# Kernel optimization log

Measured on AMD Instinct MI355X. Metric: run time of the kernel, lower is better.

## Reference

```python
import jax, jax.numpy as jnp
import numpy as np

N = 4096
IN_F = 128
OUT_F = 128
H = 4
D = OUT_F // H  # head_out = 32
SLOPE = 0.2
LN_EPS = 1e-5


def setup_inputs() -> dict:
    key = jax.random.key(0)
    k_x, k_adj, k_W, k_a = jax.random.split(key, 4)
    x = jax.random.normal(k_x, (N, IN_F), dtype=jnp.float32)
    adjacency = jax.random.randint(k_adj, (N, N), 0, 2).astype(jnp.bool_)
    # xavier-uniform-ish init scales
    w_std = float(np.sqrt(2.0 / (IN_F + H * D)))
    a_std = float(np.sqrt(2.0 / (H + 2 * D)))
    W = jax.random.normal(k_W, (H * D, IN_F), dtype=jnp.float32) * w_std  # torch Linear weight layout
    a = jax.random.normal(k_a, (H, 2 * D), dtype=jnp.float32) * a_std
    ln_gamma = jnp.ones((OUT_F,), dtype=jnp.float32)
    ln_beta = jnp.zeros((OUT_F,), dtype=jnp.float32)
    return {"x": x, "adjacency": adjacency, "W": W, "a": a,
            "ln_gamma": ln_gamma, "ln_beta": ln_beta}


def reference(x, adjacency, W, a, ln_gamma, ln_beta):
    # Wx: (N, H, D)
    Wx = (x @ W.T).reshape(N, H, D)
    # e[i,j,h] = leaky_relu( <Wx[i,h], a[h,:D]> + <Wx[j,h], a[h,D:]> )
    # (exact factorization of the original cat([Wx_i, Wx_j]) * a sum)
    alpha_i = jnp.einsum('nhd,hd->nh', Wx, a[:, :D])  # source/i term
    alpha_j = jnp.einsum('nhd,hd->nh', Wx, a[:, D:])  # neighbor/j term
    e = alpha_i[:, None, :] + alpha_j[None, :, :]      # (N, N, H)
    e = jnp.where(e >= 0, e, SLOPE * e)                # LeakyReLU
    e = jnp.where(adjacency[:, :, None], e, -jnp.inf)  # mask non-edges
    attn = jax.nn.softmax(e, axis=1)                   # softmax over j
    out = jnp.einsum('ijh,jhd->ihd', attn, Wx).reshape(N, H * D)
    y = out + x                                        # residual (dims match)
    mu = jnp.mean(y, axis=-1, keepdims=True)
    var = jnp.mean((y - mu) ** 2, axis=-1, keepdims=True)
    return ln_gamma * (y - mu) / jnp.sqrt(var + LN_EPS) + ln_beta
```

## Files before the change

### kernel.cpp

```cpp
#include <hip/hip_runtime.h>
#include <hip/hip_bf16.h>
#include <stdint.h>

#define NN 4096
#define SLOPE 0.2f
#define LOG2E 1.44269504088896340736f

typedef float f32x4 __attribute__((ext_vector_type(4)));
typedef short s16x8 __attribute__((ext_vector_type(8)));
typedef unsigned u32x4 __attribute__((ext_vector_type(4)));

static __device__ __forceinline__ unsigned f32_to_bf16_rne(float f) {
    unsigned u = __builtin_bit_cast(unsigned, f);
    return (u + 0x7FFFu + ((u >> 16) & 1u)) >> 16;
}

__global__ __launch_bounds__(256) void k01(const unsigned* __restrict__ adj_raw,
                                           const float* __restrict__ x,
                                           const float* __restrict__ W,
                                           const float* __restrict__ a,
                                           unsigned* __restrict__ bits,
                                           unsigned* __restrict__ wxb8,
                                           float* __restrict__ ai_s,
                                           float* __restrict__ ajT_s) {
    const int t = threadIdx.x;
    if (blockIdx.x < 2048) {
        __shared__ int s_i32;
        if (t == 0) {
            int all_small = 1;
            for (int i = 0; i < 32; ++i) all_small &= (adj_raw[i] <= 1u);
            s_i32 = all_small;
        }
        __syncthreads();
        const long o = (long)blockIdx.x * 256 + t;
        unsigned mm = 0;
        if (s_i32) {
            const u32x4* p = (const u32x4*)adj_raw + o * 8;
            #pragma unroll
            for (int g = 0; g < 8; ++g) {
                u32x4 v = p[g];
                mm |= (v.x & 1u) << (g * 4) | (v.y & 1u) << (g * 4 + 1) |
                      (v.z & 1u) << (g * 4 + 2) | (v.w & 1u) << (g * 4 + 3);
            }
        } else {
            const u32x4* p = (const u32x4*)adj_raw + o * 2;
            #pragma unroll
            for (int g = 0; g < 2; ++g) {
                u32x4 v = p[g];
                unsigned d[4] = {v.x, v.y, v.z, v.w};
                #pragma unroll
                for (int qq = 0; qq < 4; ++qq)
                    #pragma unroll
                    for (int b = 0; b < 4; ++b)
                        mm |= ((d[qq] >> (8 * b)) & 1u) << (g * 16 + qq * 4 + b);
            }
        }
        bits[o] = mm;
        return;
    }

    __shared__ unsigned short WL[128 * 136];
    __shared__ unsigned short XL[16 * 136];
    __shared__ float WxF[16 * 132];

    const int bid = blockIdx.x - 2048;
    const int i0 = bid * 16;

    for (int p4 = t; p4 < 4096; p4 += 256) {
        f32x4 w4 = *(const f32x4*)(W + 4 * p4);
        unsigned lo = f32_to_bf16_rne(w4.x) | (f32_to_bf16_rne(w4.y) << 16);
        unsigned hi = f32_to_bf16_rne(w4.z) | (f32_to_bf16_rne(w4.w) << 16);
        int c = (4 * p4) >> 7, k = (4 * p4) & 127;
        *(unsigned long long*)&WL[c * 136 + k] =
            (unsigned long long)lo | ((unsigned long long)hi << 32);
    }
    for (int p4 = t; p4 < 512; p4 += 256) {
        f32x4 x4 = *(const f32x4*)(x + (long)i0 * 128 + 4 * p4);
        unsigned lo = f32_to_bf16_rne(x4.x) | (f32_to_bf16_rne(x4.y) << 16);
        unsigned hi = f32_to_bf16_rne(x4.z) | (f32_to_bf16_rne(x4.w) << 16);
        int r = (4 * p4) >> 7, k = (4 * p4) & 127;
        *(unsigned long long*)&XL[r * 136 + k] =
            (unsigned long long)lo | ((unsigned long long)hi << 32);
    }
    __syncthreads();

    const int w = t >> 6, l = t & 63, m = l & 15, q = l >> 4;
    f32x4 acc0 = {0.f, 0.f, 0.f, 0.f}, acc1 = {0.f, 0.f, 0.f, 0.f};
    #pragma unroll
    for (int ks = 0; ks < 4; ++ks) {
        s16x8 af = *(const s16x8*)&XL[m * 136 + ks * 32 + q * 8];
        s16x8 b0 = *(const s16x8*)&WL[(w * 32 + m) * 136 + ks * 32 + q * 8];
        s16x8 b1 = *(const s16x8*)&WL[(w * 32 + 16 + m) * 136 + ks * 32 + q * 8];
        acc0 = __builtin_amdgcn_mfma_f32_16x16x32_bf16(af, b0, acc0, 0, 0, 0);
        acc1 = __builtin_amdgcn_mfma_f32_16x16x32_bf16(af, b1, acc1, 0, 0, 0);
    }
    const int jblk = i0 >> 5;
    const int qp = ((i0 & 16) + q * 4) >> 3;
    const int ehalf = q & 1;
    #pragma unroll
    for (int j2 = 0; j2 < 2; ++j2) {
        f32x4 acc = j2 ? acc1 : acc0;
        unsigned u = (unsigned)__builtin_amdgcn_cvt_pk_fp8_f32(acc[0], acc[1], 0, false);
        u = (unsigned)__builtin_amdgcn_cvt_pk_fp8_f32(acc[2], acc[3], (int)u, true);
        wxb8[(((jblk * 4 + w) * 64 + qp * 16 + m) << 2) + j2 * 2 + ehalf] = u;
        #pragma unroll
        for (int reg = 0; reg < 4; ++reg)
            WxF[(q * 4 + reg) * 132 + (2 * w + j2) * 16 + m] = acc[reg];
    }
    __syncthreads();
    if (t < 64) {
        int r = t >> 2, h = t & 3;
        float s_i = 0.f, s_j = 0.f;
        const float* ar = a + h * 64;
        #pragma unroll
        for (int d = 0; d < 32; ++d) {
            float wv = WxF[r * 132 + h * 32 + d];
            s_i += wv * ar[d];
            s_j += wv * ar[32 + d];
        }
        ai_s[(i0 + r) * 4 + h] = s_i * LOG2E;
        ajT_s[h * NN + i0 + r] = s_j * LOG2E;
    }
}

__global__ __launch_bounds__(1024, 4) void k2_attn(
        const float* __restrict__ x,
        const unsigned* __restrict__ adjbits,
        const unsigned* __restrict__ wxb8,
        const float* __restrict__ ai_s,
        const float* __restrict__ ajT_s,
        const float* __restrict__ gamma,
        const float* __restrict__ beta,
        float* __restrict__ out) {
    __shared__ float ajL[4][4096];
    __shared__ unsigned maskL[16][132];
    __shared__ float C_lds[4][16][32];
    __shared__ float l_lds[4][16];

    const int t = threadIdx.x;
    const int i0 = blockIdx.x * 16;
    const int w = t >> 6, l = t & 63;
    const int h = w & 3, p = w >> 2;
    const int m = l & 15, q = l >> 4;

    {
        const f32x4* src = (const f32x4*)ajT_s;
        f32x4* dst = (f32x4*)&ajL[0][0];
        #pragma unroll
        for (int g = 0; g < 4; ++g) dst[t + 1024 * g] = src[t + 1024 * g];
    }
    {
        #pragma unroll
        for (int g = 0; g < 2; ++g) {
            int idx = t + 1024 * g;
            int r = idx >> 7, c = idx & 127;
            maskL[r][c] = adjbits[(long)(i0 + r) * 128 + c];
        }
    }
    const float ai = ai_s[(i0 + m) * 4 + h];
    __syncthreads();

    const unsigned* bp8 = wxb8 + ((h * 64 + l) << 2);
    const float* ajh = &ajL[h][0] + q * 8;
    const long ONESB = 0x3838383838383838L;

    f32x4 acc0 = {0.f, 0.f, 0.f, 0.f}, acc1 = {0.f, 0.f, 0.f, 0.f};
    f32x4 accl = {0.f, 0.f, 0.f, 0.f};

    u32x4 bv = *(const u32x4*)(bp8 + (p << 10));
    for (int ks = p; ks < 128; ks += 4) {
        const int ksn = (ks + 4 < 128) ? (ks + 4) : ks;
        u32x4 bvn = *(const u32x4*)(bp8 + (ksn << 10));

        unsigned mq = (maskL[m][ks] >> (q * 8)) & 0xffu;
        f32x4 aj0 = *(const f32x4*)(ajh + ks * 32);
        f32x4 aj1 = *(const f32x4*)(ajh + ks * 32 + 4);

        float ev[8];
        #pragma unroll
        for (int e = 0; e < 8; ++e) {
            float s = ai + (e < 4 ? aj0[e] : aj1[e - 4]);
            s = fmaxf(s, SLOPE * s);
            float ex = __builtin_amdgcn_exp2f(s);
            ev[e] = ((mq >> e) & 1u) ? ex : 0.0f;
        }
        unsigned d0 = (unsigned)__builtin_amdgcn_cvt_pk_bf8_f32(ev[0], ev[1], 0, false);
        d0 = (unsigned)__builtin_amdgcn_cvt_pk_bf8_f32(ev[2], ev[3], (int)d0, true);
        unsigned d1 = (unsigned)__builtin_amdgcn_cvt_pk_bf8_f32(ev[4], ev[5], 0, false);
        d1 = (unsigned)__builtin_amdgcn_cvt_pk_bf8_f32(ev[6], ev[7], (int)d1, true);
        long av = (long)(((unsigned long long)d1 << 32) | d0);
        long b0 = (long)(((unsigned long long)bv.y << 32) | bv.x);
        long b1 = (long)(((unsigned long long)bv.w << 32) | bv.z);

        acc0 = __builtin_amdgcn_mfma_f32_16x16x32_bf8_fp8(av, b0, acc0, 0, 0, 0);
        acc1 = __builtin_amdgcn_mfma_f32_16x16x32_bf8_fp8(av, b1, acc1, 0, 0, 0);
        accl = __builtin_amdgcn_mfma_f32_16x16x32_bf8_fp8(av, ONESB, accl, 0, 0, 0);
        bv = bvn;
    }

    if (p == 0) {
        #pragma unroll
        for (int reg = 0; reg < 4; ++reg) {
            C_lds[h][q * 4 + reg][m] = acc0[reg];
            C_lds[h][q * 4 + reg][16 + m] = acc1[reg];
            if (m == 0) l_lds[h][q * 4 + reg] = accl[reg];
        }
    }
    __syncthreads();
    if (p == 1) {
        #pragma unroll
        for (int reg = 0; reg < 4; ++reg) {
            C_lds[h][q * 4 + reg][m] += acc0[reg];
            C_lds[h][q * 4 + reg][16 + m] += acc1[reg];
            if (m == 0) l_lds[h][q * 4 + reg] += accl[reg];
        }
    }
    __syncthreads();
    if (p == 2) {
        #pragma unroll
        for (int reg = 0; reg < 4; ++reg) {
            C_lds[h][q * 4 + reg][m] += acc0[reg];
            C_lds[h][q * 4 + reg][16 + m] += acc1[reg];
            if (m == 0) l_lds[h][q * 4 + reg] += accl[reg];
        }
    }
    __syncthreads();
    if (p == 3) {
        #pragma unroll
        for (int reg = 0; reg < 4; ++reg) {
            C_lds[h][q * 4 + reg][m] += acc0[reg];
            C_lds[h][q * 4 + reg][16 + m] += acc1[reg];
            if (m == 0) l_lds[h][q * 4 + reg] += accl[reg];
        }
    }
    __syncthreads();

    if (t < 512) {
        const int r = t >> 5, c32 = t & 31;
        const int f0 = c32 * 4;
        const int hh = f0 >> 5, cl = f0 & 31;
        const float linv = 1.0f / l_lds[hh][r];
        f32x4 xv = *(const f32x4*)(x + (long)(i0 + r) * 128 + f0);
        float y[4], s1 = 0.f, s2 = 0.f;
        #pragma unroll
        for (int kk = 0; kk < 4; ++kk) {
            float yy = C_lds[hh][r][cl + kk] * linv + xv[kk];
            y[kk] = yy; s1 += yy; s2 += yy * yy;
        }
        #pragma unroll
        for (int s = 1; s <= 16; s <<= 1) {
            s1 += __shfl_xor(s1, s, 64);
            s2 += __shfl_xor(s2, s, 64);
        }
        const float mean = s1 * (1.0f / 128.0f);
        const float var = s2 * (1.0f / 128.0f) - mean * mean;
        const float rstd = rsqrtf(var + 1e-5f);
        f32x4 gv = *(const f32x4*)(gamma + f0);
        f32x4 bv2 = *(const f32x4*)(beta + f0);
        f32x4 ov;
        #pragma unroll
        for (int kk = 0; kk < 4; ++kk)
            ov[kk] = gv[kk] * ((y[kk] - mean) * rstd) + bv2[kk];
        *(f32x4*)(out + (long)(i0 + r) * 128 + f0) = ov;
    }
}

extern "C" void kernel_launch(void* const* d_in, const int* in_sizes, int n_in,
                              void* d_out, int out_size, void* d_ws, size_t ws_size,
                              hipStream_t stream) {
    const float* x = (const float*)d_in[0];
    const unsigned* adj_raw = (const unsigned*)d_in[1];
    const float* W = (const float*)d_in[2];
    const float* a = (const float*)d_in[3];
    const float* gamma = (const float*)d_in[4];
    const float* beta = (const float*)d_in[5];

    unsigned* wxb8 = (unsigned*)d_ws;
    float* ai_s = (float*)((char*)d_ws + (512 << 10));
    float* ajT_s = (float*)((char*)d_ws + (576 << 10));
    unsigned* adjbits = (unsigned*)((char*)d_ws + (1 << 20));

    k01<<<2304, 256, 0, stream>>>(adj_raw, x, W, a, adjbits, wxb8, ai_s, ajT_s);
    k2_attn<<<256, 1024, 0, stream>>>(x, adjbits, wxb8, ai_s, ajT_s, gamma, beta,
                                      (float*)d_out);
}
```

Before: 135.4 us.

## Factor exp of LeakyReLU into per-node exponentials and fuse adjacency packing into attention

The attention kernel no longer evaluates exp2 per edge. Since exp(leaky(a+b)) = max(exp(a)exp(b), exp(0.2a)exp(0.2b)), the per-node exponentials are computed once in the Wx kernel, and the inner loop only does half-precision multiplies and a max. The adjacency bit-packing pass is removed from the first kernel, and the attention kernel now reads the raw adjacency directly, staging it chunk by chunk into LDS. Wx and the attention weights move from fp8/bf8 to fp16 MFMA, which doubles B-operand traffic but gains precision. The product of exponentials in fp16 can overflow or underflow, because there is no max-subtraction.

Result: slower. 146.1 us (+7.9%).

```diff
diff --git a/kernel.cpp b/kernel.cpp
--- a/kernel.cpp
+++ b/kernel.cpp
@@ -1,9 +1,9 @@
 #include <hip/hip_runtime.h>
 #include <hip/hip_bf16.h>
+#include <hip/hip_fp16.h>
 #include <stdint.h>
 
 #define NN 4096
-#define SLOPE 0.2f
 #define LOG2E 1.44269504088896340736f
 
 typedef float f32x4 __attribute__((ext_vector_type(4)));
@@ -15,56 +15,18 @@
     return (u + 0x7FFFu + ((u >> 16) & 1u)) >> 16;
 }
 
-__global__ __launch_bounds__(256) void k01(const unsigned* __restrict__ adj_raw,
-                                           const float* __restrict__ x,
-                                           const float* __restrict__ W,
-                                           const float* __restrict__ a,
-                                           unsigned* __restrict__ bits,
-                                           unsigned* __restrict__ wxb8,
-                                           float* __restrict__ ai_s,
-                                           float* __restrict__ ajT_s) {
-    const int t = threadIdx.x;
-    if (blockIdx.x < 2048) {
-        __shared__ int s_i32;
-        if (t == 0) {
-            int all_small = 1;
-            for (int i = 0; i < 32; ++i) all_small &= (adj_raw[i] <= 1u);
-            s_i32 = all_small;
-        }
-        __syncthreads();
-        const long o = (long)blockIdx.x * 256 + t;
-        unsigned mm = 0;
-        if (s_i32) {
-            const u32x4* p = (const u32x4*)adj_raw + o * 8;
-            #pragma unroll
-            for (int g = 0; g < 8; ++g) {
-                u32x4 v = p[g];
-                mm |= (v.x & 1u) << (g * 4) | (v.y & 1u) << (g * 4 + 1) |
-                      (v.z & 1u) << (g * 4 + 2) | (v.w & 1u) << (g * 4 + 3);
-            }
-        } else {
-            const u32x4* p = (const u32x4*)adj_raw + o * 2;
-            #pragma unroll
-            for (int g = 0; g < 2; ++g) {
-                u32x4 v = p[g];
-                unsigned d[4] = {v.x, v.y, v.z, v.w};
-                #pragma unroll
-                for (int qq = 0; qq < 4; ++qq)
-                    #pragma unroll
-                    for (int b = 0; b < 4; ++b)
-                        mm |= ((d[qq] >> (8 * b)) & 1u) << (g * 16 + qq * 4 + b);
-            }
-        }
-        bits[o] = mm;
-        return;
-    }
-
+__global__ __launch_bounds__(256) void k1_wx(const float* __restrict__ x,
+                                             const float* __restrict__ W,
+                                             const float* __restrict__ a,
+                                             unsigned* __restrict__ wxb16,
+                                             float* __restrict__ ai_s,
+                                             unsigned* __restrict__ ejfj) {
     __shared__ unsigned short WL[128 * 136];
     __shared__ unsigned short XL[16 * 136];
     __shared__ float WxF[16 * 132];
 
-    const int bid = blockIdx.x - 2048;
-    const int i0 = bid * 16;
+    const int t = threadIdx.x;
+    const int i0 = blockIdx.x * 16;
 
     for (int p4 = t; p4 < 4096; p4 += 256) {
         f32x4 w4 = *(const f32x4*)(W + 4 * p4);
@@ -95,17 +57,20 @@
         acc1 = __builtin_amdgcn_mfma_f32_16x16x32_bf16(af, b1, acc1, 0, 0, 0);
     }
     const int jblk = i0 >> 5;
-    const int qp = ((i0 & 16) + q * 4) >> 3;
-    const int ehalf = q & 1;
+    const int qslot = ((i0 & 16) + q * 4) >> 3;
+    const int dhalf = q & 1;
     #pragma unroll
     for (int j2 = 0; j2 < 2; ++j2) {
+        const int fblk = 2 * w + j2;
         f32x4 acc = j2 ? acc1 : acc0;
-        unsigned u = (unsigned)__builtin_amdgcn_cvt_pk_fp8_f32(acc[0], acc[1], 0, false);
-        u = (unsigned)__builtin_amdgcn_cvt_pk_fp8_f32(acc[2], acc[3], (int)u, true);
-        wxb8[(((jblk * 4 + w) * 64 + qp * 16 + m) << 2) + j2 * 2 + ehalf] = u;
+        __half2 h01 = __floats2half2_rn(acc[0], acc[1]);
+        __half2 h23 = __floats2half2_rn(acc[2], acc[3]);
+        unsigned* wp = wxb16 + (((jblk * 8 + fblk) * 64 + qslot * 16 + m) << 2) + dhalf * 2;
+        wp[0] = __builtin_bit_cast(unsigned, h01);
+        wp[1] = __builtin_bit_cast(unsigned, h23);
         #pragma unroll
         for (int reg = 0; reg < 4; ++reg)
-            WxF[(q * 4 + reg) * 132 + (2 * w + j2) * 16 + m] = acc[reg];
+            WxF[(q * 4 + reg) * 132 + fblk * 16 + m] = acc[reg];
     }
     __syncthreads();
     if (t < 64) {
@@ -119,20 +84,21 @@
             s_j += wv * ar[32 + d];
         }
         ai_s[(i0 + r) * 4 + h] = s_i * LOG2E;
-        ajT_s[h * NN + i0 + r] = s_j * LOG2E;
+        float sjl = s_j * LOG2E;
+        __half2 ef = __floats2half2_rn(exp2f(sjl), exp2f(0.2f * sjl));
+        ejfj[h * NN + i0 + r] = __builtin_bit_cast(unsigned, ef);
     }
 }
 
 __global__ __launch_bounds__(1024, 4) void k2_attn(
         const float* __restrict__ x,
-        const unsigned* __restrict__ adjbits,
-        const unsigned* __restrict__ wxb8,
+        const unsigned* __restrict__ adj_raw,
+        const unsigned* __restrict__ wxb16,
         const float* __restrict__ ai_s,
-        const float* __restrict__ ajT_s,
+        const unsigned* __restrict__ ejfj,
         const float* __restrict__ gamma,
         const float* __restrict__ beta,
         float* __restrict__ out) {
-    __shared__ float ajL[4][4096];
     __shared__ unsigned maskL[16][132];
     __shared__ float C_lds[4][16][32];
     __shared__ float l_lds[4][16];
@@ -142,60 +108,103 @@
     const int w = t >> 6, l = t & 63;
     const int h = w & 3, p = w >> 2;
     const int m = l & 15, q = l >> 4;
-
-    {
-        const f32x4* src = (const f32x4*)ajT_s;
-        f32x4* dst = (f32x4*)&ajL[0][0];
-        #pragma unroll
-        for (int g = 0; g < 4; ++g) dst[t + 1024 * g] = src[t + 1024 * g];
-    }
-    {
-        #pragma unroll
-        for (int g = 0; g < 2; ++g) {
-            int idx = t + 1024 * g;
-            int r = idx >> 7, c = idx & 127;
-            maskL[r][c] = adjbits[(long)(i0 + r) * 128 + c];
-        }
-    }
-    const float ai = ai_s[(i0 + m) * 4 + h];
-    __syncthreads();
-
-    const unsigned* bp8 = wxb8 + ((h * 64 + l) << 2);
-    const float* ajh = &ajL[h][0] + q * 8;
-    const long ONESB = 0x3838383838383838L;
+    const int rt = t >> 6, ct = t & 63;
+
+    unsigned dv = adj_raw[l & 31];
+    const bool is_i32 = __all(dv <= 1u) != 0;
+
+    const float aif = ai_s[(i0 + m) * 4 + h];
+    const __half2 eifi = __floats2half2_rn(exp2f(aif), exp2f(0.2f * aif));
+
+    const unsigned* bbase = wxb16 + ((2 * h) * 64 + l) * 4;
+    const unsigned* efbase = ejfj + h * NN + q * 8;
+    const s16x8 ONESH = {0x3C00, 0x3C00, 0x3C00, 0x3C00,
+                         0x3C00, 0x3C00, 0x3C00, 0x3C00};
 
     f32x4 acc0 = {0.f, 0.f, 0.f, 0.f}, acc1 = {0.f, 0.f, 0.f, 0.f};
     f32x4 accl = {0.f, 0.f, 0.f, 0.f};
 
-    u32x4 bv = *(const u32x4*)(bp8 + (p << 10));
-    for (int ks = p; ks < 128; ks += 4) {
-        const int ksn = (ks + 4 < 128) ? (ks + 4) : ks;
-        u32x4 bvn = *(const u32x4*)(bp8 + (ksn << 10));
-
-        unsigned mq = (maskL[m][ks] >> (q * 8)) & 0xffu;
-        f32x4 aj0 = *(const f32x4*)(ajh + ks * 32);
-        f32x4 aj1 = *(const f32x4*)(ajh + ks * 32 + 4);
-
-        float ev[8];
-        #pragma unroll
-        for (int e = 0; e < 8; ++e) {
-            float s = ai + (e < 4 ? aj0[e] : aj1[e - 4]);
-            s = fmaxf(s, SLOPE * s);
-            float ex = __builtin_amdgcn_exp2f(s);
-            ev[e] = ((mq >> e) & 1u) ? ex : 0.0f;
-        }
-        unsigned d0 = (unsigned)__builtin_amdgcn_cvt_pk_bf8_f32(ev[0], ev[1], 0, false);
-        d0 = (unsigned)__builtin_amdgcn_cvt_pk_bf8_f32(ev[2], ev[3], (int)d0, true);
-        unsigned d1 = (unsigned)__builtin_amdgcn_cvt_pk_bf8_f32(ev[4], ev[5], 0, false);
-        d1 = (unsigned)__builtin_amdgcn_cvt_pk_bf8_f32(ev[6], ev[7], (int)d1, true);
-        long av = (long)(((unsigned long long)d1 << 32) | d0);
-        long b0 = (long)(((unsigned long long)bv.y << 32) | bv.x);
-        long b1 = (long)(((unsigned long long)bv.w << 32) | bv.z);
-
-        acc0 = __builtin_amdgcn_mfma_f32_16x16x32_bf8_fp8(av, b0, acc0, 0, 0, 0);
-        acc1 = __builtin_amdgcn_mfma_f32_16x16x32_bf8_fp8(av, b1, acc1, 0, 0, 0);
-        accl = __builtin_amdgcn_mfma_f32_16x16x32_bf8_fp8(av, ONESB, accl, 0, 0, 0);
-        bv = bvn;
+    u32x4 r0, r1, r2, r3;
+    {
+        if (is_i32) {
+            const u32x4* ps = (const u32x4*)(adj_raw + (long)(i0 + rt) * NN + ct * 16);
+            r0 = ps[0]; r1 = ps[1]; r2 = ps[2]; r3 = ps[3];
+        } else {
+            const u32x4* ps = (const u32x4*)((const unsigned char*)adj_raw +
+                                             (long)(i0 + rt) * NN + ct * 16);
+            r0 = ps[0];
+        }
+    }
+
+    for (int c = 0; c < 4; ++c) {
+        unsigned b;
+        if (is_i32) {
+            b = (r0.x & 1u) | ((r0.y & 1u) << 1) | ((r0.z & 1u) << 2) | ((r0.w & 1u) << 3) |
+                ((r1.x & 1u) << 4) | ((r1.y & 1u) << 5) | ((r1.z & 1u) << 6) | ((r1.w & 1u) << 7) |
+                ((r2.x & 1u) << 8) | ((r2.y & 1u) << 9) | ((r2.z & 1u) << 10) | ((r2.w & 1u) << 11) |
+                ((r3.x & 1u) << 12) | ((r3.y & 1u) << 13) | ((r3.z & 1u) << 14) | ((r3.w & 1u) << 15);
+        } else {
+            unsigned n0 = (((r0.x & 0x01010101u) * 0x08040201u) >> 24) & 0xFu;
+            unsigned n1 = (((r0.y & 0x01010101u) * 0x08040201u) >> 24) & 0xFu;
+            unsigned n2 = (((r0.z & 0x01010101u) * 0x08040201u) >> 24) & 0xFu;
+            unsigned n3 = (((r0.w & 0x01010101u) * 0x08040201u) >> 24) & 0xFu;
+            b = n0 | (n1 << 4) | (n2 << 8) | (n3 << 12);
+        }
+        {
+            unsigned short* mh = (unsigned short*)&maskL[0][0];
+            mh[(rt * 132 + c * 32 + (ct >> 1)) * 2 + (ct & 1)] = (unsigned short)b;
+        }
+        if (c < 3) {
+            if (is_i32) {
+                const u32x4* ps = (const u32x4*)(adj_raw + (long)(i0 + rt) * NN +
+                                                 (c + 1) * 1024 + ct * 16);
+                r0 = ps[0]; r1 = ps[1]; r2 = ps[2]; r3 = ps[3];
+            } else {
+                const u32x4* ps = (const u32x4*)((const unsigned char*)adj_raw +
+                                                 (long)(i0 + rt) * NN + (c + 1) * 1024 + ct * 16);
+                r0 = ps[0];
+            }
+        }
+        __syncthreads();
+
+        int ks = c * 32 + p;
+        u32x4 bva = *(const u32x4*)(bbase + ks * 2048);
+        u32x4 bvb = *(const u32x4*)(bbase + ks * 2048 + 256);
+        u32x4 efa = *(const u32x4*)(efbase + ks * 32);
+        u32x4 efb = *(const u32x4*)(efbase + ks * 32 + 4);
+
+        for (int it = 0; it < 8; ++it) {
+            int ksn = ks + 4; if (ksn > 127) ksn = ks;
+            u32x4 bva_n = *(const u32x4*)(bbase + ksn * 2048);
+            u32x4 bvb_n = *(const u32x4*)(bbase + ksn * 2048 + 256);
+            u32x4 efa_n = *(const u32x4*)(efbase + ksn * 32);
+            u32x4 efb_n = *(const u32x4*)(efbase + ksn * 32 + 4);
+
+            unsigned mq = (maskL[m][ks] >> (q * 8)) & 0xffu;
+
+            unsigned eu[8] = {efa.x, efa.y, efa.z, efa.w, efb.x, efb.y, efb.z, efb.w};
+            unsigned short ph[8];
+            #pragma unroll
+            for (int e = 0; e < 8; ++e) {
+                __half2 pr = __hmul2(eifi, __builtin_bit_cast(__half2, eu[e]));
+                __half pm = __hmax(__low2half(pr), __high2half(pr));
+                ph[e] = ((mq >> e) & 1u) ? __half_as_ushort(pm) : (unsigned short)0;
+            }
+            union { s16x8 v; unsigned u[4]; } af;
+            af.u[0] = (unsigned)ph[0] | ((unsigned)ph[1] << 16);
+            af.u[1] = (unsigned)ph[2] | ((unsigned)ph[3] << 16);
+            af.u[2] = (unsigned)ph[4] | ((unsigned)ph[5] << 16);
+            af.u[3] = (unsigned)ph[6] | ((unsigned)ph[7] << 16);
+
+            union { u32x4 u; s16x8 s; } b0c, b1c;
+            b0c.u = bva; b1c.u = bvb;
+            acc0 = __builtin_amdgcn_mfma_f32_16x16x32_f16(af.v, b0c.s, acc0, 0, 0, 0);
+            acc1 = __builtin_amdgcn_mfma_f32_16x16x32_f16(af.v, b1c.s, acc1, 0, 0, 0);
+            accl = __builtin_amdgcn_mfma_f32_16x16x32_f16(af.v, ONESH, accl, 0, 0, 0);
+
+            bva = bva_n; bvb = bvb_n; efa = efa_n; efb = efb_n;
+            ks += 4;
+        }
     }
 
     if (p == 0) {
@@ -275,12 +284,11 @@
     const float* gamma = (const float*)d_in[4];
     const float* beta = (const float*)d_in[5];
 
-    unsigned* wxb8 = (unsigned*)d_ws;
-    float* ai_s = (float*)((char*)d_ws + (512 << 10));
-    float* ajT_s = (float*)((char*)d_ws + (576 << 10));
-    unsigned* adjbits = (unsigned*)((char*)d_ws + (1 << 20));
-
-    k01<<<2304, 256, 0, stream>>>(adj_raw, x, W, a, adjbits, wxb8, ai_s, ajT_s);
-    k2_attn<<<256, 1024, 0, stream>>>(x, adjbits, wxb8, ai_s, ajT_s, gamma, beta,
+    unsigned* wxb16 = (unsigned*)d_ws;
+    float* ai_s = (float*)((char*)d_ws + (1 << 20));
+    unsigned* ejfj = (unsigned*)((char*)d_ws + (1 << 20) + (64 << 10));
+
+    k1_wx<<<256, 256, 0, stream>>>(x, W, a, wxb16, ai_s, ejfj);
+    k2_attn<<<256, 1024, 0, stream>>>(x, adj_raw, wxb16, ai_s, ejfj, gamma, beta,
                                       (float*)d_out);
 }
```
